# Kernel tuning notes

Measured on AMD Instinct MI355X. Metric: run time of the kernel, lower is better.

The kernel has to match this reference:

```python
import jax, jax.numpy as jnp
import numpy as np

# Adjacent1d: locally-connected 1D op with per-output-position unshared weights.
# out[b, oc, os] = sum_{ic, k} x[b, ic, start(os)+k] * W[ic, k, oc, os] + bias[oc, os]
# where start(os) = floor(os * in_s / out_s). With in_s = out_s * kernel_size the
# windows tile the input exactly (matches the assert in_s/kernel_size <= out_s).

B, IN_C, IN_S = 4, 64, 16384
OUT_C, OUT_S = 64, 4096
K = 4


def setup_inputs() -> dict:
    key = jax.random.key(0)
    k1, k2, k3 = jax.random.split(key, 3)
    x = jax.random.normal(k1, (B, IN_C, IN_S), dtype=jnp.float32)
    weights = jax.random.normal(k2, (IN_C, K, OUT_C, OUT_S), dtype=jnp.float32) * 0.05
    bias = jax.random.normal(k3, (OUT_C, OUT_S), dtype=jnp.float32) * 0.05
    return {"x": x, "weights": weights, "bias": bias}


def reference(x, weights, bias):
    in_s = x.shape[-1]
    out_s = weights.shape[-1]
    k = weights.shape[1]
    # window start per output position (proportional mapping)
    starts = (jnp.arange(out_s) * in_s) // out_s          # [out_s]
    idx = starts[:, None] + jnp.arange(k)[None, :]        # [out_s, K]
    idx = jnp.minimum(idx, in_s - 1)                      # safety clamp (no-op when in_s = out_s*K)
    gathered = x[:, :, idx]                               # [B, in_c, out_s, K]
    # contract over input channels and kernel taps with per-position weights
    out = jnp.einsum('bisk,ikos->bos', gathered, weights) # [B, out_c, out_s]
    return out + bias[None, :, :]
```

## Files before the change

### kernel.cpp

```cpp
#include <hip/hip_runtime.h>


#define IN_C_  64
#define OUT_S_LOG2 12

__global__ __launch_bounds__(256) void adj1d_kernel(
    const float* __restrict__ x, const float* __restrict__ w,
    const float* __restrict__ bias, float* __restrict__ out) {

  int bid = blockIdx.x;
  int wgid = (bid & 7) * 64 + (bid >> 3);
  int og = wgid & 31;
  int st = wgid >> 5;
  int s  = (st << 8) + threadIdx.x;
  int o0 = og << 1;

  float acc00 = 0.f, acc01 = 0.f, acc02 = 0.f, acc03 = 0.f;
  float acc10 = 0.f, acc11 = 0.f, acc12 = 0.f, acc13 = 0.f;

  const float4* __restrict__ xv = reinterpret_cast<const float4*>(x);
  const float* __restrict__ wp0 = w + (o0 << OUT_S_LOG2) + s;

  #pragma unroll 2
  for (int i = 0; i < IN_C_; ++i) {
    float xa[4][4];
    *reinterpret_cast<float4*>(xa[0]) = xv[((0 * IN_C_ + i) << 12) + s];
    *reinterpret_cast<float4*>(xa[1]) = xv[((1 * IN_C_ + i) << 12) + s];
    *reinterpret_cast<float4*>(xa[2]) = xv[((2 * IN_C_ + i) << 12) + s];
    *reinterpret_cast<float4*>(xa[3]) = xv[((3 * IN_C_ + i) << 12) + s];
    #pragma unroll
    for (int k = 0; k < 4; ++k) {
      const float* wp = wp0 + (size_t)(i * 4 + k) * 262144;
      float wa = __builtin_nontemporal_load(wp);
      float wb = __builtin_nontemporal_load(wp + 4096);
      acc00 = fmaf(xa[0][k], wa, acc00);
      acc01 = fmaf(xa[1][k], wa, acc01);
      acc02 = fmaf(xa[2][k], wa, acc02);
      acc03 = fmaf(xa[3][k], wa, acc03);
      acc10 = fmaf(xa[0][k], wb, acc10);
      acc11 = fmaf(xa[1][k], wb, acc11);
      acc12 = fmaf(xa[2][k], wb, acc12);
      acc13 = fmaf(xa[3][k], wb, acc13);
    }
  }

  float bA = bias[(o0 << OUT_S_LOG2) + s];
  float bB = bias[((o0 + 1) << OUT_S_LOG2) + s];

  __builtin_nontemporal_store(acc00 + bA, &out[((0 * 64 + o0) << OUT_S_LOG2) + s]);
  __builtin_nontemporal_store(acc01 + bA, &out[((1 * 64 + o0) << OUT_S_LOG2) + s]);
  __builtin_nontemporal_store(acc02 + bA, &out[((2 * 64 + o0) << OUT_S_LOG2) + s]);
  __builtin_nontemporal_store(acc03 + bA, &out[((3 * 64 + o0) << OUT_S_LOG2) + s]);
  __builtin_nontemporal_store(acc10 + bB, &out[((0 * 64 + o0 + 1) << OUT_S_LOG2) + s]);
  __builtin_nontemporal_store(acc11 + bB, &out[((1 * 64 + o0 + 1) << OUT_S_LOG2) + s]);
  __builtin_nontemporal_store(acc12 + bB, &out[((2 * 64 + o0 + 1) << OUT_S_LOG2) + s]);
  __builtin_nontemporal_store(acc13 + bB, &out[((3 * 64 + o0 + 1) << OUT_S_LOG2) + s]);
}

extern "C" void kernel_launch(void* const* d_in, const int* in_sizes, int n_in,
                              void* d_out, int out_size, void* d_ws, size_t ws_size,
                              hipStream_t stream) {
  const float* x    = (const float*)d_in[0];
  const float* w    = (const float*)d_in[1];
  const float* bias = (const float*)d_in[2];
  float* out = (float*)d_out;

  adj1d_kernel<<<512, 256, 0, stream>>>(x, w, bias, out);
}
```

Before: 65.96 us.

## Remap threads to batch×position with 8 output channels per thread

Each block now covers 64 positions for 4 batches (one wavefront per batch) and each thread computes 8 output channels instead of 2 channels × 4 batches. All four wavefronts in a block read the same weights, so weight loads are shared through cache, and each x float4 now feeds 8 channels. The nontemporal hints on weight loads and output stores are dropped in favour of plain accesses. Each wavefront now reads only 64 consecutive floats per weight row (256 bytes), and the weight reuse depends on the four wavefronts hitting cache at about the same time.

```diff
diff --git a/kernel.cpp b/kernel.cpp
--- a/kernel.cpp
+++ b/kernel.cpp
@@ -1,8 +1,5 @@
 #include <hip/hip_runtime.h>
 
-
-#define IN_C_  64
-#define OUT_S_LOG2 12
 
 __global__ __launch_bounds__(256) void adj1d_kernel(
     const float* __restrict__ x, const float* __restrict__ w,
@@ -10,51 +7,39 @@
 
   int bid = blockIdx.x;
   int wgid = (bid & 7) * 64 + (bid >> 3);
-  int og = wgid & 31;
-  int st = wgid >> 5;
-  int s  = (st << 8) + threadIdx.x;
-  int o0 = og << 1;
+  int og = wgid & 7;
+  int st = wgid >> 3;
+  int lane = threadIdx.x & 63;
+  int b = threadIdx.x >> 6;
+  int s = (st << 6) + lane;
+  int o0 = og << 3;
 
-  float acc00 = 0.f, acc01 = 0.f, acc02 = 0.f, acc03 = 0.f;
-  float acc10 = 0.f, acc11 = 0.f, acc12 = 0.f, acc13 = 0.f;
+  float acc[8];
+  #pragma unroll
+  for (int o = 0; o < 8; ++o) acc[o] = 0.f;
 
   const float4* __restrict__ xv = reinterpret_cast<const float4*>(x);
-  const float* __restrict__ wp0 = w + (o0 << OUT_S_LOG2) + s;
+  const float* __restrict__ wp0 = w + (o0 << 12) + s;
 
   #pragma unroll 2
-  for (int i = 0; i < IN_C_; ++i) {
-    float xa[4][4];
-    *reinterpret_cast<float4*>(xa[0]) = xv[((0 * IN_C_ + i) << 12) + s];
-    *reinterpret_cast<float4*>(xa[1]) = xv[((1 * IN_C_ + i) << 12) + s];
-    *reinterpret_cast<float4*>(xa[2]) = xv[((2 * IN_C_ + i) << 12) + s];
-    *reinterpret_cast<float4*>(xa[3]) = xv[((3 * IN_C_ + i) << 12) + s];
+  for (int i = 0; i < 64; ++i) {
+    float4 xa4 = xv[(((b << 6) + i) << 12) + s];
+    const float xa[4] = {xa4.x, xa4.y, xa4.z, xa4.w};
     #pragma unroll
     for (int k = 0; k < 4; ++k) {
       const float* wp = wp0 + (size_t)(i * 4 + k) * 262144;
-      float wa = __builtin_nontemporal_load(wp);
-      float wb = __builtin_nontemporal_load(wp + 4096);
-      acc00 = fmaf(xa[0][k], wa, acc00);
-      acc01 = fmaf(xa[1][k], wa, acc01);
-      acc02 = fmaf(xa[2][k], wa, acc02);
-      acc03 = fmaf(xa[3][k], wa, acc03);
-      acc10 = fmaf(xa[0][k], wb, acc10);
-      acc11 = fmaf(xa[1][k], wb, acc11);
-      acc12 = fmaf(xa[2][k], wb, acc12);
-      acc13 = fmaf(xa[3][k], wb, acc13);
+      #pragma unroll
+      for (int o = 0; o < 8; ++o) {
+        acc[o] = fmaf(xa[k], wp[o << 12], acc[o]);
+      }
     }
   }
 
-  float bA = bias[(o0 << OUT_S_LOG2) + s];
-  float bB = bias[((o0 + 1) << OUT_S_LOG2) + s];
-
-  __builtin_nontemporal_store(acc00 + bA, &out[((0 * 64 + o0) << OUT_S_LOG2) + s]);
-  __builtin_nontemporal_store(acc01 + bA, &out[((1 * 64 + o0) << OUT_S_LOG2) + s]);
-  __builtin_nontemporal_store(acc02 + bA, &out[((2 * 64 + o0) << OUT_S_LOG2) + s]);
-  __builtin_nontemporal_store(acc03 + bA, &out[((3 * 64 + o0) << OUT_S_LOG2) + s]);
-  __builtin_nontemporal_store(acc10 + bB, &out[((0 * 64 + o0 + 1) << OUT_S_LOG2) + s]);
-  __builtin_nontemporal_store(acc11 + bB, &out[((1 * 64 + o0 + 1) << OUT_S_LOG2) + s]);
-  __builtin_nontemporal_store(acc12 + bB, &out[((2 * 64 + o0 + 1) << OUT_S_LOG2) + s]);
-  __builtin_nontemporal_store(acc13 + bB, &out[((3 * 64 + o0 + 1) << OUT_S_LOG2) + s]);
+  #pragma unroll
+  for (int o = 0; o < 8; ++o) {
+    float bv = bias[((o0 + o) << 12) + s];
+    out[(((b << 6) + o0 + o) << 12) + s] = acc[o] + bv;
+  }
 }
 
 extern "C" void kernel_launch(void* const* d_in, const int* in_sizes, int n_in,
```

Result: slower. 176.3 us (+167.2%).
